# Kernel tuning notes

Measured on AMD Instinct MI355X. Metric: run time of the kernel, lower is better.

The kernel has to match this reference:

```python
import jax, jax.numpy as jnp
import numpy as np

B, S, D, H = 2, 2048, 1024, 16
DK = D // H


def setup_inputs() -> dict:
    key = jax.random.key(0)
    ks = jax.random.split(key, 12)
    scale = 1.0 / np.sqrt(D)
    inp = {
        "Q": jax.random.normal(ks[0], (B, S, D), jnp.float32),
        "K": jax.random.normal(ks[1], (B, S, D), jnp.float32),
        "V": jax.random.normal(ks[2], (B, S, D), jnp.float32),
        # causal mask, broadcastable to [B, H, S, S]; 0 -> masked
        "Mask": jnp.tril(jnp.ones((S, S), jnp.int32))[None, None],
        "Wq": jax.random.normal(ks[3], (D, D), jnp.float32) * scale,
        "bq": jnp.zeros((D,), jnp.float32),
        "Wk": jax.random.normal(ks[4], (D, D), jnp.float32) * scale,
        "bk": jnp.zeros((D,), jnp.float32),
        "Wv": jax.random.normal(ks[5], (D, D), jnp.float32) * scale,
        "bv": jnp.zeros((D,), jnp.float32),
        "Wo": jax.random.normal(ks[6], (D, D), jnp.float32) * scale,
        "bo": jnp.zeros((D,), jnp.float32),
    }
    return inp


def _heads(x):
    # [B, S, D] -> [B, H, S, DK]
    return x.reshape(B, S, H, DK).transpose(0, 2, 1, 3)


def reference(Q, K, V, Mask, Wq, bq, Wk, bk, Wv, bv, Wo, bo):
    q = _heads(Q @ Wq.T + bq)
    k = _heads(K @ Wk.T + bk)
    v = _heads(V @ Wv.T + bv)
    # NOTE: original module does NOT scale by 1/sqrt(d_k)
    logits = jnp.einsum("bhqd,bhkd->bhqk", q, k)
    logits = jnp.where(Mask == 0, jnp.float32(-1e9), logits)
    attn = jax.nn.softmax(logits, axis=-1)  # dropout p=0.0 -> identity
    ctx = jnp.einsum("bhqk,bhkd->bhqd", attn, v)
    ctx = ctx.transpose(0, 2, 1, 3).reshape(B, S, D)
    return ctx @ Wo.T + bo
```

## Files before the change

kernel.cpp:

```cpp
#include <hip/hip_runtime.h>
#include <hip/hip_bf16.h>

#define B_  2
#define S_  2048
#define D_  1024
#define H_  16
#define DK_ 64
#define M_  (B_ * S_)

typedef __bf16 bf16;
typedef __bf16 bf16x8 __attribute__((ext_vector_type(8)));
typedef __bf16 bf16x4 __attribute__((ext_vector_type(4)));
typedef float  f32x4  __attribute__((ext_vector_type(4)));

#define MFMA16(a, b, c) __builtin_amdgcn_mfma_f32_16x16x32_bf16((a), (b), (c), 0, 0, 0)

__device__ __forceinline__ void gl2lds16(const bf16* g, bf16* l) {
    __builtin_amdgcn_global_load_lds((const __attribute__((address_space(1))) void*)g,
                                     (__attribute__((address_space(3))) void*)l, 16, 0, 0);
}

struct CastArgs { const float* src[7]; bf16* dst[7]; };

__global__ __launch_bounds__(256) void cast_all(CastArgs a) {
    int i = blockIdx.x * 256 + threadIdx.x;
    int seg, off;
    if (i < 3145728) { seg = i >> 20; off = i & 1048575; }
    else { int j = i - 3145728; seg = 3 + (j >> 18); off = j & 262143; }
    float4 v = ((const float4*)a.src[seg])[off];
    bf16x4 o;
    o[0] = (bf16)v.x; o[1] = (bf16)v.y; o[2] = (bf16)v.z; o[3] = (bf16)v.w;
    *(bf16x4*)&a.dst[seg][(size_t)off * 4] = o;
}

__device__ __forceinline__ void gemm_core(const bf16* __restrict__ A,
                                          const bf16* __restrict__ Bt,
                                          const float* __restrict__ bias,
                                          void* __restrict__ Out, int mode) {
    __shared__ bf16 As[128 * 32];
    __shared__ bf16 Bs[128 * 32];

    const int t = threadIdx.x, lane = t & 63, w = t >> 6;
    const int lr = lane & 15, lq = lane >> 4;
    const int wm = (w >> 1) * 64, wn = (w & 1) * 64;
    const int n0 = blockIdx.x * 128, m0 = blockIdx.y * 128;

    const int c0 = w * 128 + lane, c1 = c0 + 64;
    const bf16* Ag0 = A  + (size_t)(m0 + (c0 >> 2)) * 1024 + (c0 & 3) * 8;
    const bf16* Ag1 = A  + (size_t)(m0 + (c1 >> 2)) * 1024 + (c1 & 3) * 8;
    const bf16* Bg0 = Bt + (size_t)(n0 + (c0 >> 2)) * 1024 + (c0 & 3) * 8;
    const bf16* Bg1 = Bt + (size_t)(n0 + (c1 >> 2)) * 1024 + (c1 & 3) * 8;
    bf16* Al0 = As + (w * 128) * 8;
    bf16* Al1 = As + (w * 128 + 64) * 8;
    bf16* Bl0 = Bs + (w * 128) * 8;
    bf16* Bl1 = Bs + (w * 128 + 64) * 8;

    f32x4 acc[4][4];
#pragma unroll
    for (int mi = 0; mi < 4; ++mi)
#pragma unroll
        for (int ni = 0; ni < 4; ++ni) acc[mi][ni] = 0.0f;

    for (int k0 = 0; k0 < 1024; k0 += 32) {
        __syncthreads();
        gl2lds16(Ag0 + k0, Al0);
        gl2lds16(Ag1 + k0, Al1);
        gl2lds16(Bg0 + k0, Bl0);
        gl2lds16(Bg1 + k0, Bl1);
        __syncthreads();
        bf16x8 af[4], bfr[4];
#pragma unroll
        for (int mi = 0; mi < 4; ++mi) af[mi]  = *(const bf16x8*)&As[(wm + mi * 16 + lr) * 32 + lq * 8];
#pragma unroll
        for (int ni = 0; ni < 4; ++ni) bfr[ni] = *(const bf16x8*)&Bs[(wn + ni * 16 + lr) * 32 + lq * 8];
#pragma unroll
        for (int mi = 0; mi < 4; ++mi)
#pragma unroll
            for (int ni = 0; ni < 4; ++ni) acc[mi][ni] = MFMA16(af[mi], bfr[ni], acc[mi][ni]);
    }

#pragma unroll
    for (int mi = 0; mi < 4; ++mi) {
#pragma unroll
        for (int ni = 0; ni < 4; ++ni) {
            int gn = n0 + wn + ni * 16 + lr;
            float bv = bias[gn];
#pragma unroll
            for (int r = 0; r < 4; ++r) {
                int gm = m0 + wm + mi * 16 + lq * 4 + r;
                float v = acc[mi][ni][r] + bv;
                if (mode == 0) {
                    int b = gm >> 11, s = gm & (S_ - 1);
                    int h = gn >> 6, dk = gn & 63;
                    ((bf16*)Out)[(((size_t)(b * H_ + h) * S_ + s) << 6) + dk] = (bf16)v;
                } else if (mode == 1) {
                    int b = gm >> 11, s = gm & (S_ - 1);
                    int h = gn >> 6, dk = gn & 63;
                    ((bf16*)Out)[(((size_t)(b * H_ + h) * DK_ + dk) << 11) + s] = (bf16)v;
                } else {
                    ((float*)Out)[(size_t)gm * 1024 + gn] = v;
                }
            }
        }
    }
}

struct QkvArgs { const bf16* A[3]; const bf16* W[3]; const float* bias[3]; bf16* out[3]; };

__global__ __launch_bounds__(256, 2) void gemm_qkv(QkvArgs a) {
    int z = blockIdx.z;
    gemm_core(a.A[z], a.W[z], a.bias[z], (void*)a.out[z], z == 2 ? 1 : 0);
}

__global__ __launch_bounds__(256, 2) void gemm_out(const bf16* __restrict__ A,
                                                   const bf16* __restrict__ Bt,
                                                   const float* __restrict__ bias,
                                                   float* __restrict__ Out) {
    gemm_core(A, Bt, bias, (void*)Out, 2);
}

__global__ __launch_bounds__(256, 1) void flash_attn(const bf16* __restrict__ qh,
                                                     const bf16* __restrict__ kh,
                                                     const bf16* __restrict__ vt,
                                                     bf16* __restrict__ ctx) {
    __shared__ char smem[65536];
    bf16* Qs = (bf16*)smem;
    bf16* Ks = (bf16*)(smem + 16384);
    bf16* Ps = (bf16*)(smem + 32768);

    const int pair = blockIdx.x, h = blockIdx.y, b = blockIdx.z;
    const int bh = b * H_ + h;
    const bf16* Qp = qh + (size_t)bh * S_ * DK_;
    const bf16* Kp = kh + (size_t)bh * S_ * DK_;
    const bf16* Vp = vt + (size_t)bh * DK_ * S_;

    const int t = threadIdx.x, lane = t & 63, w = t >> 6;
    const int lr = lane & 15, lq = lane >> 4;
    const int wq = w & 1, wk = w >> 1;
    bf16* Pw = Ps + w * 4096;

    for (int half = 0; half < 2; ++half) {
        const int qt = half ? (15 - pair) : pair;

#pragma unroll
        for (int i = 0; i < 4; ++i) {
            int c = w * 256 + i * 64 + lane;
            int qrow = c >> 3, xx = (c & 7) ^ (qrow & 7);
            gl2lds16(Qp + (size_t)(qt * 128 + qrow) * 64 + xx * 8, Qs + (w * 256 + i * 64) * 8);
        }

        f32x4 oacc[4][4];
#pragma unroll
        for (int mt = 0; mt < 4; ++mt)
#pragma unroll
            for (int nt = 0; nt < 4; ++nt) oacc[mt][nt] = 0.0f;
        float lpart[4] = {0.f, 0.f, 0.f, 0.f};

        for (int kt = 0; kt <= qt; ++kt) {
            __syncthreads();
#pragma unroll
            for (int i = 0; i < 4; ++i) {
                int c = w * 256 + i * 64 + lane;
                int krow = c >> 3, xx = (c & 7) ^ (krow & 7);
                gl2lds16(Kp + (size_t)(kt * 128 + krow) * 64 + xx * 8, Ks + (w * 256 + i * 64) * 8);
            }
            __syncthreads();

            const int k64 = kt * 2 + wk, q64 = qt * 2 + wq;
            if (k64 <= q64) {
                bf16x8 bv[2][4];
#pragma unroll
                for (int kk = 0; kk < 2; ++kk)
#pragma unroll
                    for (int nt = 0; nt < 4; ++nt)
                        bv[kk][nt] = *(const bf16x8*)(Vp + (size_t)(nt * 16 + lr) * S_ +
                                                      kt * 128 + wk * 64 + kk * 32 + lq * 8);
                f32x4 s[4][4];
#pragma unroll
                for (int mt = 0; mt < 4; ++mt)
#pragma unroll
                    for (int nt = 0; nt < 4; ++nt) s[mt][nt] = 0.0f;
#pragma unroll
                for (int ks = 0; ks < 2; ++ks) {
                    bf16x8 af[4], qf[4];
                    int xx = (ks * 4 + lq) ^ (lr & 7);
#pragma unroll
                    for (int mt = 0; mt < 4; ++mt)
                        af[mt] = *(const bf16x8*)&Ks[(wk * 64 + mt * 16 + lr) * 64 + xx * 8];
#pragma unroll
                    for (int nt = 0; nt < 4; ++nt)
                        qf[nt] = *(const bf16x8*)&Qs[(wq * 64 + nt * 16 + lr) * 64 + xx * 8];
#pragma unroll
                    for (int mt = 0; mt < 4; ++mt)
#pragma unroll
                        for (int nt = 0; nt < 4; ++nt) s[mt][nt] = MFMA16(af[mt], qf[nt], s[mt][nt]);
                }
                const bool diag = (k64 == q64);
#pragma unroll
                for (int mt = 0; mt < 4; ++mt)
#pragma unroll
                    for (int nt = 0; nt < 4; ++nt) {
                        bf16x4 pb;
#pragma unroll
                        for (int r = 0; r < 4; ++r) {
                            int kl = mt * 16 + lq * 4 + r;
                            int ql = nt * 16 + lr;
                            float p = (!diag || kl <= ql) ? __expf(s[mt][nt][r]) : 0.0f;
                            bf16 p16 = (bf16)p;
                            lpart[nt] += (float)p16;
                            pb[r] = p16;
                        }
                        int xx = (2 * mt + (lq >> 1)) ^ (lr & 7);
                        *(bf16x4*)&Pw[(nt * 16 + lr) * 64 + xx * 8 + (lq & 1) * 4] = pb;
                    }
#pragma unroll
                for (int kk = 0; kk < 2; ++kk) {
                    bf16x8 ap[4];
                    int xx = (kk * 4 + lq) ^ (lr & 7);
#pragma unroll
                    for (int mt2 = 0; mt2 < 4; ++mt2)
                        ap[mt2] = *(const bf16x8*)&Pw[(mt2 * 16 + lr) * 64 + xx * 8];
#pragma unroll
                    for (int mt2 = 0; mt2 < 4; ++mt2)
#pragma unroll
                        for (int nt = 0; nt < 4; ++nt)
                            oacc[mt2][nt] = MFMA16(ap[mt2], bv[kk][nt], oacc[mt2][nt]);
                }
            }
        }

        __syncthreads();
#pragma unroll
        for (int nt = 0; nt < 4; ++nt) {
            lpart[nt] += __shfl_xor(lpart[nt], 16);
            lpart[nt] += __shfl_xor(lpart[nt], 32);
        }
        float* Op = (float*)(smem + 32768);
        float* Lh = (float*)smem;
        if (lq == 0)
#pragma unroll
            for (int nt = 0; nt < 4; ++nt) Lh[wk * 128 + wq * 64 + nt * 16 + lr] = lpart[nt];
        if (wk == 1) {
#pragma unroll
            for (int mt = 0; mt < 4; ++mt)
#pragma unroll
                for (int nt = 0; nt < 4; ++nt)
#pragma unroll
                    for (int r = 0; r < 4; ++r) {
                        int row = mt * 16 + lq * 4 + r, col = nt * 16 + lr;
                        int xx = (col >> 2) ^ (row & 15);
                        Op[wq * 4096 + row * 64 + xx * 4 + (col & 3)] = oacc[mt][nt][r];
                    }
        }
        __syncthreads();
        if (wk == 0) {
            float linv[4][4];
#pragma unroll
            for (int mt = 0; mt < 4; ++mt)
#pragma unroll
                for (int r = 0; r < 4; ++r) {
                    int qq = wq * 64 + mt * 16 + lq * 4 + r;
                    linv[mt][r] = 1.0f / (Lh[qq] + Lh[128 + qq]);
                }
#pragma unroll
            for (int mt = 0; mt < 4; ++mt)
#pragma unroll
                for (int nt = 0; nt < 4; ++nt)
#pragma unroll
                    for (int r = 0; r < 4; ++r) {
                        int row = mt * 16 + lq * 4 + r, col = nt * 16 + lr;
                        int xx = (col >> 2) ^ (row & 15);
                        float v = (oacc[mt][nt][r] + Op[wq * 4096 + row * 64 + xx * 4 + (col & 3)]) * linv[mt][r];
                        int q = qt * 128 + wq * 64 + row;
                        ctx[((size_t)(b * S_ + q)) * D_ + h * DK_ + col] = (bf16)v;
                    }
        }
        __syncthreads();
    }
}

extern "C" void kernel_launch(void* const* d_in, const int* in_sizes, int n_in,
                              void* d_out, int out_size, void* d_ws, size_t ws_size,
                              hipStream_t stream) {
    const float* Q  = (const float*)d_in[0];
    const float* K  = (const float*)d_in[1];
    const float* V  = (const float*)d_in[2];
    const float* Wq = (const float*)d_in[4];
    const float* bq = (const float*)d_in[5];
    const float* Wk = (const float*)d_in[6];
    const float* bk = (const float*)d_in[7];
    const float* Wv = (const float*)d_in[8];
    const float* bv = (const float*)d_in[9];
    const float* Wo = (const float*)d_in[10];
    const float* bo = (const float*)d_in[11];

    char* p = (char*)d_ws;
    bf16* Qb  = (bf16*)p;  p += (size_t)M_ * D_ * 2;
    bf16* Kb  = (bf16*)p;  p += (size_t)M_ * D_ * 2;
    bf16* Vb  = (bf16*)p;  p += (size_t)M_ * D_ * 2;
    bf16* Wqb = (bf16*)p;  p += (size_t)D_ * D_ * 2;
    bf16* Wkb = (bf16*)p;  p += (size_t)D_ * D_ * 2;
    bf16* Wvb = (bf16*)p;  p += (size_t)D_ * D_ * 2;
    bf16* Wob = (bf16*)p;  p += (size_t)D_ * D_ * 2;
    bf16* qhd = (bf16*)p;  p += (size_t)M_ * D_ * 2;
    bf16* khd = (bf16*)p;  p += (size_t)M_ * D_ * 2;
    bf16* vtr = (bf16*)p;  p += (size_t)M_ * D_ * 2;
    bf16* ctx = (bf16*)p;  p += (size_t)M_ * D_ * 2;

    CastArgs ca;
    ca.src[0] = Q;  ca.dst[0] = Qb;
    ca.src[1] = K;  ca.dst[1] = Kb;
    ca.src[2] = V;  ca.dst[2] = Vb;
    ca.src[3] = Wq; ca.dst[3] = Wqb;
    ca.src[4] = Wk; ca.dst[4] = Wkb;
    ca.src[5] = Wv; ca.dst[5] = Wvb;
    ca.src[6] = Wo; ca.dst[6] = Wob;
    cast_all<<<16384, 256, 0, stream>>>(ca);

    QkvArgs qa;
    qa.A[0] = Qb;  qa.A[1] = Kb;  qa.A[2] = Vb;
    qa.W[0] = Wqb; qa.W[1] = Wkb; qa.W[2] = Wvb;
    qa.bias[0] = bq; qa.bias[1] = bk; qa.bias[2] = bv;
    qa.out[0] = qhd; qa.out[1] = khd; qa.out[2] = vtr;
    dim3 qgrid(D_ / 128, M_ / 128, 3);
    gemm_qkv<<<qgrid, 256, 0, stream>>>(qa);

    dim3 fgrid(8, H_, B_);
    flash_attn<<<fgrid, 256, 0, stream>>>(qhd, khd, vtr, ctx);

    dim3 ogrid(D_ / 128, M_ / 128);
    gemm_out<<<ogrid, 256, 0, stream>>>(ctx, Wob, bo, (float*)d_out);
}
```

Measured before the change: 251.8 us.

## Shrink attention query tiles and output GEMM tiles to raise block count and occupancy

Flash attention now processes 64-query tiles against 128-key tiles, doubling the grid to 16x16x2 blocks, cutting shared memory to 40KB and allowing 2 blocks per CU. The output projection GEMM gets its own kernel with 64x128 tiles, doubling its block count. The QKV GEMM is specialized and its launch bound raised to 3 blocks per CU. The goal is to fill the 256 CUs better, at the cost of more K/V reloads per query and less reuse per block.

```diff
diff --git a/kernel.cpp b/kernel.cpp
--- a/kernel.cpp
+++ b/kernel.cpp
@@ -33,12 +33,18 @@
     *(bf16x4*)&a.dst[seg][(size_t)off * 4] = o;
 }
 
-__device__ __forceinline__ void gemm_core(const bf16* __restrict__ A,
-                                          const bf16* __restrict__ Bt,
-                                          const float* __restrict__ bias,
-                                          void* __restrict__ Out, int mode) {
+struct QkvArgs { const bf16* A[3]; const bf16* W[3]; const float* bias[3]; bf16* out[3]; };
+
+__global__ __launch_bounds__(256, 3) void gemm_qkv(QkvArgs ar) {
     __shared__ bf16 As[128 * 32];
     __shared__ bf16 Bs[128 * 32];
+
+    const int z = blockIdx.z;
+    const bf16* A  = ar.A[z];
+    const bf16* Bt = ar.W[z];
+    const float* bias = ar.bias[z];
+    bf16* Out = ar.out[z];
+    const int mode = (z == 2) ? 1 : 0;
 
     const int t = threadIdx.x, lane = t & 63, w = t >> 6;
     const int lr = lane & 15, lq = lane >> 4;
@@ -89,44 +95,84 @@
             for (int r = 0; r < 4; ++r) {
                 int gm = m0 + wm + mi * 16 + lq * 4 + r;
                 float v = acc[mi][ni][r] + bv;
-                if (mode == 0) {
-                    int b = gm >> 11, s = gm & (S_ - 1);
-                    int h = gn >> 6, dk = gn & 63;
-                    ((bf16*)Out)[(((size_t)(b * H_ + h) * S_ + s) << 6) + dk] = (bf16)v;
-                } else if (mode == 1) {
-                    int b = gm >> 11, s = gm & (S_ - 1);
-                    int h = gn >> 6, dk = gn & 63;
-                    ((bf16*)Out)[(((size_t)(b * H_ + h) * DK_ + dk) << 11) + s] = (bf16)v;
-                } else {
-                    ((float*)Out)[(size_t)gm * 1024 + gn] = v;
-                }
+                int b = gm >> 11, s = gm & (S_ - 1);
+                int h = gn >> 6, dk = gn & 63;
+                if (mode == 0)
+                    Out[(((size_t)(b * H_ + h) * S_ + s) << 6) + dk] = (bf16)v;
+                else
+                    Out[(((size_t)(b * H_ + h) * DK_ + dk) << 11) + s] = (bf16)v;
             }
         }
     }
-}
-
-struct QkvArgs { const bf16* A[3]; const bf16* W[3]; const float* bias[3]; bf16* out[3]; };
-
-__global__ __launch_bounds__(256, 2) void gemm_qkv(QkvArgs a) {
-    int z = blockIdx.z;
-    gemm_core(a.A[z], a.W[z], a.bias[z], (void*)a.out[z], z == 2 ? 1 : 0);
 }
 
 __global__ __launch_bounds__(256, 2) void gemm_out(const bf16* __restrict__ A,
                                                    const bf16* __restrict__ Bt,
                                                    const float* __restrict__ bias,
                                                    float* __restrict__ Out) {
-    gemm_core(A, Bt, bias, (void*)Out, 2);
-}
-
-__global__ __launch_bounds__(256, 1) void flash_attn(const bf16* __restrict__ qh,
+    __shared__ bf16 As[64 * 32];
+    __shared__ bf16 Bs[128 * 32];
+
+    const int t = threadIdx.x, lane = t & 63, w = t >> 6;
+    const int lr = lane & 15, lq = lane >> 4;
+    const int wm = (w >> 1) * 32, wn = (w & 1) * 64;
+    const int n0 = blockIdx.x * 128, m0 = blockIdx.y * 64;
+
+    const int ca = w * 64 + lane;
+    const int cb0 = w * 128 + lane, cb1 = cb0 + 64;
+    const bf16* Ag  = A  + (size_t)(m0 + (ca >> 2)) * 1024 + (ca & 3) * 8;
+    const bf16* Bg0 = Bt + (size_t)(n0 + (cb0 >> 2)) * 1024 + (cb0 & 3) * 8;
+    const bf16* Bg1 = Bt + (size_t)(n0 + (cb1 >> 2)) * 1024 + (cb1 & 3) * 8;
+    bf16* Al  = As + (w * 64) * 8;
+    bf16* Bl0 = Bs + (w * 128) * 8;
+    bf16* Bl1 = Bs + (w * 128 + 64) * 8;
+
+    f32x4 acc[2][4];
+#pragma unroll
+    for (int mi = 0; mi < 2; ++mi)
+#pragma unroll
+        for (int ni = 0; ni < 4; ++ni) acc[mi][ni] = 0.0f;
+
+    for (int k0 = 0; k0 < 1024; k0 += 32) {
+        __syncthreads();
+        gl2lds16(Ag + k0, Al);
+        gl2lds16(Bg0 + k0, Bl0);
+        gl2lds16(Bg1 + k0, Bl1);
+        __syncthreads();
+        bf16x8 af[2], bfr[4];
+#pragma unroll
+        for (int mi = 0; mi < 2; ++mi) af[mi]  = *(const bf16x8*)&As[(wm + mi * 16 + lr) * 32 + lq * 8];
+#pragma unroll
+        for (int ni = 0; ni < 4; ++ni) bfr[ni] = *(const bf16x8*)&Bs[(wn + ni * 16 + lr) * 32 + lq * 8];
+#pragma unroll
+        for (int mi = 0; mi < 2; ++mi)
+#pragma unroll
+            for (int ni = 0; ni < 4; ++ni) acc[mi][ni] = MFMA16(af[mi], bfr[ni], acc[mi][ni]);
+    }
+
+#pragma unroll
+    for (int mi = 0; mi < 2; ++mi) {
+#pragma unroll
+        for (int ni = 0; ni < 4; ++ni) {
+            int gn = n0 + wn + ni * 16 + lr;
+            float bv = bias[gn];
+#pragma unroll
+            for (int r = 0; r < 4; ++r) {
+                int gm = m0 + wm + mi * 16 + lq * 4 + r;
+                Out[(size_t)gm * 1024 + gn] = acc[mi][ni][r] + bv;
+            }
+        }
+    }
+}
+
+__global__ __launch_bounds__(256, 2) void flash_attn(const bf16* __restrict__ qh,
                                                      const bf16* __restrict__ kh,
                                                      const bf16* __restrict__ vt,
                                                      bf16* __restrict__ ctx) {
-    __shared__ char smem[65536];
+    __shared__ char smem[40960];
     bf16* Qs = (bf16*)smem;
-    bf16* Ks = (bf16*)(smem + 16384);
-    bf16* Ps = (bf16*)(smem + 32768);
+    bf16* Ks = (bf16*)(smem + 8192);
+    bf16* Ps = (bf16*)(smem + 24576);
 
     const int pair = blockIdx.x, h = blockIdx.y, b = blockIdx.z;
     const int bh = b * H_ + h;
@@ -137,26 +183,27 @@
     const int t = threadIdx.x, lane = t & 63, w = t >> 6;
     const int lr = lane & 15, lq = lane >> 4;
     const int wq = w & 1, wk = w >> 1;
-    bf16* Pw = Ps + w * 4096;
+    bf16* Pw = Ps + w * 2048;
 
     for (int half = 0; half < 2; ++half) {
-        const int qt = half ? (15 - pair) : pair;
-
-#pragma unroll
-        for (int i = 0; i < 4; ++i) {
-            int c = w * 256 + i * 64 + lane;
+        const int qt = half ? (31 - pair) : pair;
+
+#pragma unroll
+        for (int i = 0; i < 2; ++i) {
+            int c = w * 128 + i * 64 + lane;
             int qrow = c >> 3, xx = (c & 7) ^ (qrow & 7);
-            gl2lds16(Qp + (size_t)(qt * 128 + qrow) * 64 + xx * 8, Qs + (w * 256 + i * 64) * 8);
-        }
-
-        f32x4 oacc[4][4];
-#pragma unroll
-        for (int mt = 0; mt < 4; ++mt)
+            gl2lds16(Qp + (size_t)(qt * 64 + qrow) * 64 + xx * 8, Qs + (w * 128 + i * 64) * 8);
+        }
+
+        f32x4 oacc[2][4];
+#pragma unroll
+        for (int mt = 0; mt < 2; ++mt)
 #pragma unroll
             for (int nt = 0; nt < 4; ++nt) oacc[mt][nt] = 0.0f;
-        float lpart[4] = {0.f, 0.f, 0.f, 0.f};
-
-        for (int kt = 0; kt <= qt; ++kt) {
+        float lpart[2] = {0.f, 0.f};
+
+        const int nkt = qt / 2 + 1;
+        for (int kt = 0; kt < nkt; ++kt) {
             __syncthreads();
 #pragma unroll
             for (int i = 0; i < 4; ++i) {
@@ -166,8 +213,8 @@
             }
             __syncthreads();
 
-            const int k64 = kt * 2 + wk, q64 = qt * 2 + wq;
-            if (k64 <= q64) {
+            const int k64 = kt * 2 + wk;
+            if (k64 <= qt) {
                 bf16x8 bv[2][4];
 #pragma unroll
                 for (int kk = 0; kk < 2; ++kk)
@@ -175,37 +222,37 @@
                     for (int nt = 0; nt < 4; ++nt)
                         bv[kk][nt] = *(const bf16x8*)(Vp + (size_t)(nt * 16 + lr) * S_ +
                                                       kt * 128 + wk * 64 + kk * 32 + lq * 8);
-                f32x4 s[4][4];
+                f32x4 s[4][2];
 #pragma unroll
                 for (int mt = 0; mt < 4; ++mt)
 #pragma unroll
-                    for (int nt = 0; nt < 4; ++nt) s[mt][nt] = 0.0f;
+                    for (int nt = 0; nt < 2; ++nt) s[mt][nt] = 0.0f;
 #pragma unroll
                 for (int ks = 0; ks < 2; ++ks) {
-                    bf16x8 af[4], qf[4];
+                    bf16x8 af[4], qf[2];
                     int xx = (ks * 4 + lq) ^ (lr & 7);
 #pragma unroll
                     for (int mt = 0; mt < 4; ++mt)
                         af[mt] = *(const bf16x8*)&Ks[(wk * 64 + mt * 16 + lr) * 64 + xx * 8];
 #pragma unroll
-                    for (int nt = 0; nt < 4; ++nt)
-                        qf[nt] = *(const bf16x8*)&Qs[(wq * 64 + nt * 16 + lr) * 64 + xx * 8];
+                    for (int nt = 0; nt < 2; ++nt)
+                        qf[nt] = *(const bf16x8*)&Qs[(wq * 32 + nt * 16 + lr) * 64 + xx * 8];
 #pragma unroll
                     for (int mt = 0; mt < 4; ++mt)
 #pragma unroll
-                        for (int nt = 0; nt < 4; ++nt) s[mt][nt] = MFMA16(af[mt], qf[nt], s[mt][nt]);
+                        for (int nt = 0; nt < 2; ++nt) s[mt][nt] = MFMA16(af[mt], qf[nt], s[mt][nt]);
                 }
-                const bool diag = (k64 == q64);
+                const bool diag = (k64 == qt);
 #pragma unroll
                 for (int mt = 0; mt < 4; ++mt)
 #pragma unroll
-                    for (int nt = 0; nt < 4; ++nt) {
+                    for (int nt = 0; nt < 2; ++nt) {
                         bf16x4 pb;
 #pragma unroll
                         for (int r = 0; r < 4; ++r) {
                             int kl = mt * 16 + lq * 4 + r;
-                            int ql = nt * 16 + lr;
-                            float p = (!diag || kl <= ql) ? __expf(s[mt][nt][r]) : 0.0f;
+                            int qlT = wq * 32 + nt * 16 + lr;
+                            float p = (!diag || kl <= qlT) ? __expf(s[mt][nt][r]) : 0.0f;
                             bf16 p16 = (bf16)p;
                             lpart[nt] += (float)p16;
                             pb[r] = p16;
@@ -215,13 +262,13 @@
                     }
 #pragma unroll
                 for (int kk = 0; kk < 2; ++kk) {
-                    bf16x8 ap[4];
+                    bf16x8 ap[2];
                     int xx = (kk * 4 + lq) ^ (lr & 7);
 #pragma unroll
-                    for (int mt2 = 0; mt2 < 4; ++mt2)
+                    for (int mt2 = 0; mt2 < 2; ++mt2)
                         ap[mt2] = *(const bf16x8*)&Pw[(mt2 * 16 + lr) * 64 + xx * 8];
 #pragma unroll
-                    for (int mt2 = 0; mt2 < 4; ++mt2)
+                    for (int mt2 = 0; mt2 < 2; ++mt2)
 #pragma unroll
                         for (int nt = 0; nt < 4; ++nt)
                             oacc[mt2][nt] = MFMA16(ap[mt2], bv[kk][nt], oacc[mt2][nt]);
@@ -231,47 +278,47 @@
 
         __syncthreads();
 #pragma unroll
-        for (int nt = 0; nt < 4; ++nt) {
+        for (int nt = 0; nt < 2; ++nt) {
             lpart[nt] += __shfl_xor(lpart[nt], 16);
             lpart[nt] += __shfl_xor(lpart[nt], 32);
         }
-        float* Op = (float*)(smem + 32768);
+        float* Op = (float*)(smem + 24576);
         float* Lh = (float*)smem;
         if (lq == 0)
 #pragma unroll
-            for (int nt = 0; nt < 4; ++nt) Lh[wk * 128 + wq * 64 + nt * 16 + lr] = lpart[nt];
+            for (int nt = 0; nt < 2; ++nt) Lh[wk * 64 + wq * 32 + nt * 16 + lr] = lpart[nt];
         if (wk == 1) {
 #pragma unroll
-            for (int mt = 0; mt < 4; ++mt)
+            for (int mt = 0; mt < 2; ++mt)
 #pragma unroll
                 for (int nt = 0; nt < 4; ++nt)
 #pragma unroll
                     for (int r = 0; r < 4; ++r) {
                         int row = mt * 16 + lq * 4 + r, col = nt * 16 + lr;
                         int xx = (col >> 2) ^ (row & 15);
-                        Op[wq * 4096 + row * 64 + xx * 4 + (col & 3)] = oacc[mt][nt][r];
+                        Op[wq * 2048 + row * 64 + xx * 4 + (col & 3)] = oacc[mt][nt][r];
                     }
         }
         __syncthreads();
         if (wk == 0) {
-            float linv[4][4];
-#pragma unroll
-            for (int mt = 0; mt < 4; ++mt)
+            float linv[2][4];
+#pragma unroll
+            for (int mt = 0; mt < 2; ++mt)
 #pragma unroll
                 for (int r = 0; r < 4; ++r) {
-                    int qq = wq * 64 + mt * 16 + lq * 4 + r;
-                    linv[mt][r] = 1.0f / (Lh[qq] + Lh[128 + qq]);
+                    int qq = wq * 32 + mt * 16 + lq * 4 + r;
+                    linv[mt][r] = 1.0f / (Lh[qq] + Lh[64 + qq]);
                 }
 #pragma unroll
-            for (int mt = 0; mt < 4; ++mt)
+            for (int mt = 0; mt < 2; ++mt)
 #pragma unroll
                 for (int nt = 0; nt < 4; ++nt)
 #pragma unroll
                     for (int r = 0; r < 4; ++r) {
                         int row = mt * 16 + lq * 4 + r, col = nt * 16 + lr;
                         int xx = (col >> 2) ^ (row & 15);
-                        float v = (oacc[mt][nt][r] + Op[wq * 4096 + row * 64 + xx * 4 + (col & 3)]) * linv[mt][r];
-                        int q = qt * 128 + wq * 64 + row;
+                        float v = (oacc[mt][nt][r] + Op[wq * 2048 + row * 64 + xx * 4 + (col & 3)]) * linv[mt][r];
+                        int q = qt * 64 + wq * 32 + row;
                         ctx[((size_t)(b * S_ + q)) * D_ + h * DK_ + col] = (bf16)v;
                     }
         }
@@ -325,9 +372,9 @@
     dim3 qgrid(D_ / 128, M_ / 128, 3);
     gemm_qkv<<<qgrid, 256, 0, stream>>>(qa);
 
-    dim3 fgrid(8, H_, B_);
+    dim3 fgrid(16, H_, B_);
     flash_attn<<<fgrid, 256, 0, stream>>>(qhd, khd, vtr, ctx);
 
-    dim3 ogrid(D_ / 128, M_ / 128);
+    dim3 ogrid(D_ / 128, M_ / 64);
     gemm_out<<<ogrid, 256, 0, stream>>>(ctx, Wob, bo, (float*)d_out);
 }
```

Result: faster. 240.6 us (-4.4%).
